# Kernel tuning notes

Measured on AMD Instinct MI355X. Metric: run time of the kernel, lower is better.

The kernel has to match this reference:

```python
import jax, jax.numpy as jnp
import numpy as np

N = 200000
IN_CH = 128
HIDDEN = [512, 512, 256]
NUM_TYPES = 10


def hetero_linear(x, types, W, b):
    # y[n] = x[n] @ W[types[n]] + b[types[n]]
    # Loop over the small fixed set of types (grouped GEMM as masked dense GEMMs).
    out = jnp.zeros((x.shape[0], W.shape[2]), dtype=x.dtype)
    for t in range(W.shape[0]):
        yt = x @ W[t] + b[t]
        out = out + jnp.where((types == t)[:, None], yt, jnp.zeros((), x.dtype))
    return out


def setup_inputs() -> dict:
    key = jax.random.key(0)
    ks = jax.random.split(key, 8)
    dims = [IN_CH] + HIDDEN
    inp = {
        "x": jax.random.normal(ks[0], (N, IN_CH), dtype=jnp.float32),
        "atom_types": jax.random.randint(ks[1], (N,), 0, NUM_TYPES, dtype=jnp.int32),
    }
    for i in range(3):
        fan_in = dims[i]
        scale = 1.0 / np.sqrt(fan_in)
        inp[f"W{i}"] = jax.random.normal(ks[2 + 2 * i], (NUM_TYPES, dims[i], dims[i + 1]), dtype=jnp.float32) * scale
        inp[f"b{i}"] = jax.random.normal(ks[3 + 2 * i], (NUM_TYPES, dims[i + 1]), dtype=jnp.float32) * scale
    return inp


def reference(x, atom_types, W0, b0, W1, b1, W2, b2):
    h = jax.nn.relu(hetero_linear(x, atom_types, W0, b0))
    h = jax.nn.relu(hetero_linear(h, atom_types, W1, b1))
    return hetero_linear(h, atom_types, W2, b2)
```

## Files before the change

### kernel.cpp

```cpp
#include <hip/hip_runtime.h>
#include <stdint.h>

typedef float  f32x4  __attribute__((ext_vector_type(4)));
typedef short  bf16x8 __attribute__((ext_vector_type(8)));

#define TYPES 10
#define D_IN  128
#define D_H1  512
#define D_H2  512
#define D_OUT 256

__device__ __forceinline__ unsigned short f2bf(float f) {
  union { float f; unsigned u; } v; v.f = f;
  unsigned u = v.u;
  return (unsigned short)((u + 0x7FFFu + ((u >> 16) & 1u)) >> 16);
}

__device__ __forceinline__ void async16(void* lds, const void* g) {
  __builtin_amdgcn_global_load_lds(
      (const __attribute__((address_space(1))) void*)g,
      (__attribute__((address_space(3))) void*)lds, 16, 0, 0);
}

__global__ void k_init(int* meta) {
  if (threadIdx.x < 48) meta[threadIdx.x] = 0;
}

__global__ void k_hist(const int* __restrict__ types, int n, int* __restrict__ meta) {
  __shared__ int lc[TYPES];
  if (threadIdx.x < TYPES) lc[threadIdx.x] = 0;
  __syncthreads();
  int i = blockIdx.x * 256 + threadIdx.x;
  if (i < n) atomicAdd(&lc[types[i]], 1);
  __syncthreads();
  if (threadIdx.x < TYPES && lc[threadIdx.x]) atomicAdd(&meta[threadIdx.x], lc[threadIdx.x]);
}

__global__ void k_scan(int* meta) {
  if (threadIdx.x == 0) {
    int off = 0;
    for (int t = 0; t < TYPES; ++t) {
      meta[16 + t] = off;
      off += ((meta[t] + 255) >> 8) << 8;
    }
    meta[26] = off;
  }
}

__global__ void k_scatter(const int* __restrict__ types, int n,
                          int* __restrict__ meta, int* __restrict__ perm) {
  __shared__ int lc[TYPES], lbase[TYPES];
  if (threadIdx.x < TYPES) lc[threadIdx.x] = 0;
  __syncthreads();
  int i = blockIdx.x * 256 + threadIdx.x;
  int t = 0, loc = 0;
  bool ok = i < n;
  if (ok) { t = types[i]; loc = atomicAdd(&lc[t], 1); }
  __syncthreads();
  if (threadIdx.x < TYPES) {
    int c = lc[threadIdx.x];
    lbase[threadIdx.x] = c ? atomicAdd(&meta[32 + threadIdx.x], c) : 0;
  }
  __syncthreads();
  if (ok) perm[meta[16 + t] + lbase[t] + loc] = i;
}

__global__ void k_gather(const float* __restrict__ x, const int* __restrict__ perm,
                         const int* __restrict__ meta, unsigned short* __restrict__ xs) {
  int p = blockIdx.x * 8 + (threadIdx.x >> 5);
  if (p >= meta[26]) return;
  int t = 0;
  while (p >= meta[17 + t]) t++;
  int e = (threadIdx.x & 31) * 4;
  unsigned short o0, o1, o2, o3;
  if (p - meta[16 + t] < meta[t]) {
    const float4 v = *(const float4*)(x + (size_t)perm[p] * D_IN + e);
    o0 = f2bf(v.x); o1 = f2bf(v.y); o2 = f2bf(v.z); o3 = f2bf(v.w);
  } else {
    o0 = o1 = o2 = o3 = 0;
  }
  *(ushort4*)(xs + (size_t)p * D_IN + e) = make_ushort4(o0, o1, o2, o3);
}

__global__ void k_wtrans_all(const float* __restrict__ W0a, const float* __restrict__ W1a,
                             const float* __restrict__ W2a,
                             unsigned short* __restrict__ wt0, unsigned short* __restrict__ wt1,
                             unsigned short* __restrict__ wt2) {
  int b = blockIdx.x;
  const float* W; unsigned short* Wt; int K, NOUT, t, local;
  if (b < 160)      { W = W0a; Wt = wt0; K = 128; NOUT = 512; t = b / 16; local = b % 16; }
  else if (b < 800) { b -= 160; W = W1a; Wt = wt1; K = 512; NOUT = 512; t = b / 64; local = b % 64; }
  else              { b -= 800; W = W2a; Wt = wt2; K = 512; NOUT = 256; t = b / 32; local = b % 32; }
  int ntn = NOUT >> 6;
  int kb = local / ntn, nb = local % ntn;
  __shared__ unsigned short tile[64][65];
  const float* src = W + (size_t)t * K * NOUT + (size_t)(kb * 64) * NOUT + nb * 64;
  int c = threadIdx.x & 63;
  int r0 = threadIdx.x >> 6;
  #pragma unroll
  for (int i = 0; i < 16; ++i) {
    int r = r0 * 16 + i;
    tile[r][c] = f2bf(src[(size_t)r * NOUT + c]);
  }
  __syncthreads();
  unsigned short* dst = Wt + (size_t)t * NOUT * K + (size_t)(nb * 64) * K + kb * 64;
  #pragma unroll
  for (int i = 0; i < 16; ++i) {
    int nn = r0 * 16 + i;
    dst[(size_t)nn * K + c] = tile[c][nn];
  }
}

template <int K, int NOUT, bool RELU, bool FINAL>
__launch_bounds__(512, 2)
__global__ void k_gemm(const unsigned short* __restrict__ A,
                       const unsigned short* __restrict__ Wt,
                       const float* __restrict__ bias,
                       unsigned short* __restrict__ H,
                       float* __restrict__ OUT,
                       const int* __restrict__ meta,
                       const int* __restrict__ perm) {
  constexpr int nKT = K / 64;
  __shared__ char lds[131072];

  int NXB = gridDim.x;
  int nwg = NXB * (int)gridDim.y;
  int raw = blockIdx.x + blockIdx.y * NXB;
  int q = nwg >> 3, rr = nwg & 7;
  int xcd = raw & 7, idx = raw >> 3;
  int swz = (xcd < rr ? xcd * (q + 1) : rr * (q + 1) + (xcd - rr) * q) + idx;
  int bx = swz % NXB, by = swz / NXB;

  int row0 = by * 256;
  if (row0 >= meta[26]) return;
  int t = 0;
  while (row0 >= meta[17 + t]) t++;
  int seg = meta[16 + t], cnt = meta[t];
  int tid = threadIdx.x, lane = tid & 63, wid = tid >> 6;
  int wr = (wid >> 2) * 128, wc = (wid & 3) * 64;
  int col0 = bx * 256;
  const char* Ag = (const char*)(A + (size_t)row0 * K);
  const char* Bg = (const char*)(Wt + ((size_t)t * NOUT + col0) * K);

  int gsrc = ((tid & 7) ^ ((tid >> 3) & 7)) * 16;
  const char* aS = Ag + (size_t)(tid >> 3) * (2 * K) + gsrc;
  const char* bS = Bg + (size_t)(((tid >> 3) & 31) + ((tid >> 3) >> 5) * 64) * (2 * K) + gsrc;

  auto stage = [&](int kt, int sub) {
    if (kt >= nKT) return;
    int h = sub & 1, du = kt & 1;
    char* dst = lds + ((sub < 2) ? 0 : 65536) + (du * 2 + h) * 16384 + wid * 1024;
    const char* src = (sub < 2 ? aS + (size_t)(h * 64) * (2 * K)
                               : bS + (size_t)(h * 32) * (2 * K)) + (size_t)kt * 128;
    async16(dst,        src);
    async16(dst + 8192, src + (size_t)128 * (2 * K));
  };

  f32x4 acc[8][4] = {};
  int rA = lane & 15, qoff = (lane >> 4) * 16, xr = (lane & 7) << 4;
  int lrA = (wid >> 2) * 64;
  int clB = (wid & 3) * 32;

  stage(0, 0); stage(0, 1); stage(0, 2); stage(0, 3); stage(1, 0);
  asm volatile("s_waitcnt vmcnt(2)" ::: "memory");
  __builtin_amdgcn_s_barrier();

  for (int g = 0; g < nKT; ++g) {
    int d = g & 1;
    const char* Ad = lds + d * 32768;
    const char* Bd = lds + 65536 + d * 32768;
    bf16x8 a[4][2], b0[2][2], b1[2][2];

    #pragma unroll
    for (int m = 0; m < 4; ++m) {
      int lr = lrA + m * 16 + rA;
      #pragma unroll
      for (int kk = 0; kk < 2; ++kk)
        a[m][kk] = *(const bf16x8*)(Ad + ((lr * 128 + kk * 64 + qoff) ^ xr));
    }
    #pragma unroll
    for (int nn = 0; nn < 2; ++nn) {
      int cl = clB + nn * 16 + rA;
      #pragma unroll
      for (int kk = 0; kk < 2; ++kk) {
        b0[nn][kk] = *(const bf16x8*)(Bd +         ((cl * 128 + kk * 64 + qoff) ^ xr));
        b1[nn][kk] = *(const bf16x8*)(Bd + 16384 + ((cl * 128 + kk * 64 + qoff) ^ xr));
      }
    }
    stage(g + 1, 1); stage(g + 1, 2); stage(g + 1, 3);
    __builtin_amdgcn_s_barrier();
    asm volatile("s_waitcnt lgkmcnt(0)" ::: "memory");
    __builtin_amdgcn_s_setprio(1);
    #pragma unroll
    for (int kk = 0; kk < 2; ++kk)
      #pragma unroll
      for (int m = 0; m < 4; ++m)
        #pragma unroll
        for (int nn = 0; nn < 2; ++nn) {
          acc[m][nn]     = __builtin_amdgcn_mfma_f32_16x16x32_bf16(a[m][kk], b0[nn][kk], acc[m][nn],     0, 0, 0);
          acc[m][2 + nn] = __builtin_amdgcn_mfma_f32_16x16x32_bf16(a[m][kk], b1[nn][kk], acc[m][2 + nn], 0, 0, 0);
        }
    __builtin_amdgcn_s_setprio(0);
    __builtin_amdgcn_s_barrier();

    #pragma unroll
    for (int m = 0; m < 4; ++m) {
      int lr = lrA + m * 16 + rA;
      #pragma unroll
      for (int kk = 0; kk < 2; ++kk)
        a[m][kk] = *(const bf16x8*)(Ad + 16384 + ((lr * 128 + kk * 64 + qoff) ^ xr));
    }
    stage(g + 2, 0);
    __builtin_amdgcn_s_barrier();
    asm volatile("s_waitcnt lgkmcnt(0)" ::: "memory");
    __builtin_amdgcn_s_setprio(1);
    #pragma unroll
    for (int kk = 0; kk < 2; ++kk)
      #pragma unroll
      for (int m = 0; m < 4; ++m)
        #pragma unroll
        for (int nn = 0; nn < 2; ++nn) {
          acc[4 + m][2 + nn] = __builtin_amdgcn_mfma_f32_16x16x32_bf16(a[m][kk], b1[nn][kk], acc[4 + m][2 + nn], 0, 0, 0);
          acc[4 + m][nn]     = __builtin_amdgcn_mfma_f32_16x16x32_bf16(a[m][kk], b0[nn][kk], acc[4 + m][nn],     0, 0, 0);
        }
    __builtin_amdgcn_s_setprio(0);
    if (g + 1 < nKT) {
      if (g + 2 < nKT) asm volatile("s_waitcnt vmcnt(2)" ::: "memory");
      else             asm volatile("s_waitcnt vmcnt(0)" ::: "memory");
    }
    __builtin_amdgcn_s_barrier();
  }

  int cA = lane & 15, rE = (lane >> 4) * 4;
  float bv[4];
  #pragma unroll
  for (int ni = 0; ni < 4; ++ni) bv[ni] = bias[t * NOUT + col0 + wc + ni * 16 + cA];
  char* cb = (char*)lds;

  if (!FINAL) {
    #pragma unroll
    for (int mi = 0; mi < 8; ++mi)
      #pragma unroll
      for (int e = 0; e < 4; ++e) {
        int row = wr + mi * 16 + rE + e;
        int sw = (row & 7) << 4;
        #pragma unroll
        for (int ni = 0; ni < 4; ++ni) {
          float v = acc[mi][ni][e] + bv[ni];
          if (RELU) v = fmaxf(v, 0.f);
          int col = wc + ni * 16 + cA;
          *(unsigned short*)(cb + ((row * 512 + col * 2) ^ sw)) = f2bf(v);
        }
      }
    __builtin_amdgcn_s_barrier();
    #pragma unroll 4
    for (int r = 0; r < 16; ++r) {
      int row = wid * 32 + r * 2 + (lane >> 5);
      int addr = row * 512 + ((((lane & 31) * 16)) ^ ((row & 7) << 4));
      bf16x8 v = *(const bf16x8*)(cb + addr);
      *(bf16x8*)(H + (size_t)(row0 + row) * NOUT + col0 + (lane & 31) * 8) = v;
    }
  } else {
    int myhalf = (wid & 3) >> 1;
    #pragma unroll
    for (int p = 0; p < 2; ++p) {
      if (myhalf == p) {
        int colh = wc & 127;
        #pragma unroll
        for (int mi = 0; mi < 8; ++mi)
          #pragma unroll
          for (int e = 0; e < 4; ++e) {
            int row = wr + mi * 16 + rE + e;
            int sw = (row & 7) << 4;
            #pragma unroll
            for (int ni = 0; ni < 4; ++ni) {
              float v = acc[mi][ni][e] + bv[ni];
              if (RELU) v = fmaxf(v, 0.f);
              int col = colh + ni * 16 + cA;
              *(float*)(cb + ((row * 512 + col * 4) ^ sw)) = v;
            }
          }
      }
      __builtin_amdgcn_s_barrier();
      #pragma unroll 4
      for (int r = 0; r < 16; ++r) {
        int row = wid * 32 + r * 2 + (lane >> 5);
        int gr = row0 + row;
        int addr = row * 512 + ((((lane & 31) * 16)) ^ ((row & 7) << 4));
        float4 v = *(const float4*)(cb + addr);
        if (gr - seg < cnt) {
          int pr = perm[gr];
          *(float4*)(OUT + (size_t)pr * NOUT + p * (NOUT / 2) + (lane & 31) * 4) = v;
        }
      }
      if (p == 0) __builtin_amdgcn_s_barrier();
    }
  }
}

extern "C" void kernel_launch(void* const* d_in, const int* in_sizes, int n_in,
                              void* d_out, int out_size, void* d_ws, size_t ws_size,
                              hipStream_t stream) {
  const float* x     = (const float*)d_in[0];
  const int*   types = (const int*)d_in[1];
  const float* W0    = (const float*)d_in[2];
  const float* b0    = (const float*)d_in[3];
  const float* W1    = (const float*)d_in[4];
  const float* b1    = (const float*)d_in[5];
  const float* W2    = (const float*)d_in[6];
  const float* b2    = (const float*)d_in[7];
  float* out = (float*)d_out;
  int n = in_sizes[1];
  int RB = (n + 255) / 256 + TYPES;
  size_t NPAD = (size_t)RB * 256;

  char* ws = (char*)d_ws;
  int* meta = (int*)ws;
  int* perm = (int*)(ws + 1024);
  size_t off = 1024 + NPAD * 4;
  off = (off + 255) & ~(size_t)255;
  unsigned short* wt0 = (unsigned short*)(ws + off); off += (size_t)TYPES * D_H1 * D_IN * 2;
  unsigned short* wt1 = (unsigned short*)(ws + off); off += (size_t)TYPES * D_H2 * D_H1 * 2;
  unsigned short* wt2 = (unsigned short*)(ws + off); off += (size_t)TYPES * D_OUT * D_H2 * 2;
  off = (off + 255) & ~(size_t)255;
  unsigned short* B1 = (unsigned short*)(ws + off); off += NPAD * 512 * 2;
  unsigned short* B2 = (unsigned short*)(ws + off); off += NPAD * 512 * 2;

  int hb = (n + 255) / 256;
  k_init<<<1, 64, 0, stream>>>(meta);
  k_hist<<<hb, 256, 0, stream>>>(types, n, meta);
  k_scan<<<1, 64, 0, stream>>>(meta);
  k_scatter<<<hb, 256, 0, stream>>>(types, n, meta, perm);
  k_gather<<<RB * 32, 256, 0, stream>>>(x, perm, meta, B1);
  k_wtrans_all<<<1120, 256, 0, stream>>>(W0, W1, W2, wt0, wt1, wt2);

  k_gemm<D_IN, D_H1, true,  false><<<dim3(D_H1 / 256, RB), 512, 0, stream>>>(B1, wt0, b0, B2, nullptr, meta, perm);
  k_gemm<D_H1, D_H2, true,  false><<<dim3(D_H2 / 256, RB), 512, 0, stream>>>(B2, wt1, b1, B1, nullptr, meta, perm);
  k_gemm<D_H2, D_OUT, false, true ><<<dim3(D_OUT / 256, RB), 512, 0, stream>>>(B1, wt2, b2, nullptr, out, meta, perm);
}
```

Baseline: 433.2 us.

## Restructure GEMM main loop into four half-K phases with per-wave contiguous LDS tiles

Changes the LDS staging layout so each wave reads a contiguous 64-row A half and a 64-column B half, instead of pieces interleaved across sub-buffers. The K-step is split into four MFMA phases, each loading only four A fragments, and the next tile's staging is spread across the phases. The aim is lower register pressure and finer overlap of global-to-LDS loads with MFMA work. The cost is more barriers per iteration, and the epilogue row mapping must change to match the new accumulator ordering.

```diff
diff --git a/kernel.cpp b/kernel.cpp
--- a/kernel.cpp
+++ b/kernel.cpp
@@ -138,28 +138,27 @@
   int seg = meta[16 + t], cnt = meta[t];
   int tid = threadIdx.x, lane = tid & 63, wid = tid >> 6;
   int wr = (wid >> 2) * 128, wc = (wid & 3) * 64;
+  int ah = wid >> 2, bh = (wid & 3) >> 1, clb = (wid & 1) * 64;
   int col0 = bx * 256;
   const char* Ag = (const char*)(A + (size_t)row0 * K);
   const char* Bg = (const char*)(Wt + ((size_t)t * NOUT + col0) * K);
 
   int gsrc = ((tid & 7) ^ ((tid >> 3) & 7)) * 16;
   const char* aS = Ag + (size_t)(tid >> 3) * (2 * K) + gsrc;
-  const char* bS = Bg + (size_t)(((tid >> 3) & 31) + ((tid >> 3) >> 5) * 64) * (2 * K) + gsrc;
+  const char* bS = Bg + (size_t)(tid >> 3) * (2 * K) + gsrc;
 
   auto stage = [&](int kt, int sub) {
     if (kt >= nKT) return;
     int h = sub & 1, du = kt & 1;
     char* dst = lds + ((sub < 2) ? 0 : 65536) + (du * 2 + h) * 16384 + wid * 1024;
-    const char* src = (sub < 2 ? aS + (size_t)(h * 64) * (2 * K)
-                               : bS + (size_t)(h * 32) * (2 * K)) + (size_t)kt * 128;
+    const char* base = (sub < 2) ? aS : bS;
+    const char* src = base + (size_t)(h * 128) * (2 * K) + (size_t)kt * 128;
     async16(dst,        src);
-    async16(dst + 8192, src + (size_t)128 * (2 * K));
+    async16(dst + 8192, src + (size_t)64 * (2 * K));
   };
 
   f32x4 acc[8][4] = {};
   int rA = lane & 15, qoff = (lane >> 4) * 16, xr = (lane & 7) << 4;
-  int lrA = (wid >> 2) * 64;
-  int clB = (wid & 3) * 32;
 
   stage(0, 0); stage(0, 1); stage(0, 2); stage(0, 3); stage(1, 0);
   asm volatile("s_waitcnt vmcnt(2)" ::: "memory");
@@ -167,62 +166,82 @@
 
   for (int g = 0; g < nKT; ++g) {
     int d = g & 1;
-    const char* Ad = lds + d * 32768;
-    const char* Bd = lds + 65536 + d * 32768;
-    bf16x8 a[4][2], b0[2][2], b1[2][2];
+    const char* Au = lds + (d * 2 + ah) * 16384;
+    const char* Bu = lds + 65536 + (d * 2 + bh) * 16384;
+    bf16x8 a[4], b0[4], b1[4];
 
     #pragma unroll
     for (int m = 0; m < 4; ++m) {
-      int lr = lrA + m * 16 + rA;
-      #pragma unroll
-      for (int kk = 0; kk < 2; ++kk)
-        a[m][kk] = *(const bf16x8*)(Ad + ((lr * 128 + kk * 64 + qoff) ^ xr));
-    }
-    #pragma unroll
-    for (int nn = 0; nn < 2; ++nn) {
-      int cl = clB + nn * 16 + rA;
-      #pragma unroll
-      for (int kk = 0; kk < 2; ++kk) {
-        b0[nn][kk] = *(const bf16x8*)(Bd +         ((cl * 128 + kk * 64 + qoff) ^ xr));
-        b1[nn][kk] = *(const bf16x8*)(Bd + 16384 + ((cl * 128 + kk * 64 + qoff) ^ xr));
-      }
-    }
-    stage(g + 1, 1); stage(g + 1, 2); stage(g + 1, 3);
+      int lr = m * 16 + rA;
+      a[m] = *(const bf16x8*)(Au + lr * 128 + (qoff ^ xr));
+    }
+    #pragma unroll
+    for (int n = 0; n < 4; ++n) {
+      int cl = clb + n * 16 + rA;
+      b0[n] = *(const bf16x8*)(Bu + cl * 128 + (qoff ^ xr));
+      b1[n] = *(const bf16x8*)(Bu + cl * 128 + ((64 + qoff) ^ xr));
+    }
+    stage(g + 1, 1);
+    asm volatile("s_waitcnt lgkmcnt(8)" ::: "memory");
     __builtin_amdgcn_s_barrier();
     asm volatile("s_waitcnt lgkmcnt(0)" ::: "memory");
     __builtin_amdgcn_s_setprio(1);
     #pragma unroll
-    for (int kk = 0; kk < 2; ++kk)
-      #pragma unroll
-      for (int m = 0; m < 4; ++m)
-        #pragma unroll
-        for (int nn = 0; nn < 2; ++nn) {
-          acc[m][nn]     = __builtin_amdgcn_mfma_f32_16x16x32_bf16(a[m][kk], b0[nn][kk], acc[m][nn],     0, 0, 0);
-          acc[m][2 + nn] = __builtin_amdgcn_mfma_f32_16x16x32_bf16(a[m][kk], b1[nn][kk], acc[m][2 + nn], 0, 0, 0);
-        }
+    for (int m = 0; m < 4; ++m)
+      #pragma unroll
+      for (int n = 0; n < 4; ++n)
+        acc[m][n] = __builtin_amdgcn_mfma_f32_16x16x32_bf16(a[m], b0[n], acc[m][n], 0, 0, 0);
     __builtin_amdgcn_s_setprio(0);
     __builtin_amdgcn_s_barrier();
 
     #pragma unroll
     for (int m = 0; m < 4; ++m) {
-      int lr = lrA + m * 16 + rA;
-      #pragma unroll
-      for (int kk = 0; kk < 2; ++kk)
-        a[m][kk] = *(const bf16x8*)(Ad + 16384 + ((lr * 128 + kk * 64 + qoff) ^ xr));
-    }
-    stage(g + 2, 0);
+      int lr = m * 16 + rA;
+      a[m] = *(const bf16x8*)(Au + lr * 128 + ((64 + qoff) ^ xr));
+    }
+    stage(g + 1, 2);
     __builtin_amdgcn_s_barrier();
     asm volatile("s_waitcnt lgkmcnt(0)" ::: "memory");
     __builtin_amdgcn_s_setprio(1);
     #pragma unroll
-    for (int kk = 0; kk < 2; ++kk)
-      #pragma unroll
-      for (int m = 0; m < 4; ++m)
-        #pragma unroll
-        for (int nn = 0; nn < 2; ++nn) {
-          acc[4 + m][2 + nn] = __builtin_amdgcn_mfma_f32_16x16x32_bf16(a[m][kk], b1[nn][kk], acc[4 + m][2 + nn], 0, 0, 0);
-          acc[4 + m][nn]     = __builtin_amdgcn_mfma_f32_16x16x32_bf16(a[m][kk], b0[nn][kk], acc[4 + m][nn],     0, 0, 0);
-        }
+    for (int m = 0; m < 4; ++m)
+      #pragma unroll
+      for (int n = 0; n < 4; ++n)
+        acc[m][n] = __builtin_amdgcn_mfma_f32_16x16x32_bf16(a[m], b1[n], acc[m][n], 0, 0, 0);
+    __builtin_amdgcn_s_setprio(0);
+    __builtin_amdgcn_s_barrier();
+
+    #pragma unroll
+    for (int m = 0; m < 4; ++m) {
+      int lr = 64 + m * 16 + rA;
+      a[m] = *(const bf16x8*)(Au + lr * 128 + (qoff ^ xr));
+    }
+    stage(g + 1, 3);
+    __builtin_amdgcn_s_barrier();
+    asm volatile("s_waitcnt lgkmcnt(0)" ::: "memory");
+    __builtin_amdgcn_s_setprio(1);
+    #pragma unroll
+    for (int m = 0; m < 4; ++m)
+      #pragma unroll
+      for (int n = 0; n < 4; ++n)
+        acc[4 + m][n] = __builtin_amdgcn_mfma_f32_16x16x32_bf16(a[m], b0[n], acc[4 + m][n], 0, 0, 0);
+    __builtin_amdgcn_s_setprio(0);
+    __builtin_amdgcn_s_barrier();
+
+    #pragma unroll
+    for (int m = 0; m < 4; ++m) {
+      int lr = 64 + m * 16 + rA;
+      a[m] = *(const bf16x8*)(Au + lr * 128 + ((64 + qoff) ^ xr));
+    }
+    stage(g + 2, 0);
+    __builtin_amdgcn_s_barrier();
+    asm volatile("s_waitcnt lgkmcnt(0)" ::: "memory");
+    __builtin_amdgcn_s_setprio(1);
+    #pragma unroll
+    for (int m = 0; m < 4; ++m)
+      #pragma unroll
+      for (int n = 0; n < 4; ++n)
+        acc[4 + m][n] = __builtin_amdgcn_mfma_f32_16x16x32_bf16(a[m], b1[n], acc[4 + m][n], 0, 0, 0);
     __builtin_amdgcn_s_setprio(0);
     if (g + 1 < nKT) {
       if (g + 2 < nKT) asm volatile("s_waitcnt vmcnt(2)" ::: "memory");
@@ -239,10 +258,11 @@
 
   if (!FINAL) {
     #pragma unroll
-    for (int mi = 0; mi < 8; ++mi)
+    for (int mi = 0; mi < 8; ++mi) {
+      int rowoff = (mi >> 2) * 64 + (mi & 3) * 16;
       #pragma unroll
       for (int e = 0; e < 4; ++e) {
-        int row = wr + mi * 16 + rE + e;
+        int row = wr + rowoff + rE + e;
         int sw = (row & 7) << 4;
         #pragma unroll
         for (int ni = 0; ni < 4; ++ni) {
@@ -252,6 +272,7 @@
           *(unsigned short*)(cb + ((row * 512 + col * 2) ^ sw)) = f2bf(v);
         }
       }
+    }
     __builtin_amdgcn_s_barrier();
     #pragma unroll 4
     for (int r = 0; r < 16; ++r) {
@@ -267,10 +288,11 @@
       if (myhalf == p) {
         int colh = wc & 127;
         #pragma unroll
-        for (int mi = 0; mi < 8; ++mi)
+        for (int mi = 0; mi < 8; ++mi) {
+          int rowoff = (mi >> 2) * 64 + (mi & 3) * 16;
           #pragma unroll
           for (int e = 0; e < 4; ++e) {
-            int row = wr + mi * 16 + rE + e;
+            int row = wr + rowoff + rE + e;
             int sw = (row & 7) << 4;
             #pragma unroll
             for (int ni = 0; ni < 4; ++ni) {
@@ -280,6 +302,7 @@
               *(float*)(cb + ((row * 512 + col * 4) ^ sw)) = v;
             }
           }
+        }
       }
       __builtin_amdgcn_s_barrier();
       #pragma unroll 4
```

Measured after the change: 425.2 us, median of 2. No clear change (-1.8%).
